# Optimization experiments

Measured on AMD Instinct MI355X. Metric: run time of the kernel, lower is better.

The kernel has to match this reference:

```python
import jax, jax.numpy as jnp
import numpy as np

DT = 0.002  # hardcoded dt0 in SDE.__call__
B, T, D = 4096, 2500, 3


def setup_inputs() -> dict:
    key = jax.random.key(0)
    ks = jax.random.split(key, 6)
    # drift/diffusion scaled by 0.1 so 2500-step Euler paths stay numerically stable in fp32
    return {
        "x0": jax.random.normal(ks[0], (B, D), jnp.float32),
        "drift": jax.random.normal(ks[1], (D, D), jnp.float32) * 0.1,
        "drift_bias": jax.random.normal(ks[2], (D,), jnp.float32),
        "diffusion": jax.random.normal(ks[3], (D, D), jnp.float32) * 0.1,
        "diffusion_bias": jax.random.normal(ks[4], (D,), jnp.float32) * 0.1,
        # standard-normal Brownian increments (scaled by sqrt(dt) inside reference)
        "noise": jax.random.normal(ks[5], (T, B, D), jnp.float32),
    }


def reference(x0, drift, drift_bias, diffusion, diffusion_bias, noise):
    # Euler-Maruyama: x_{k+1} = x_k + (A x_k + b) dt + diag(C x_k + d) dW_k
    # (diag(v) @ dW == v * dW elementwise), vmapped over batch via broadcasting.
    dt = jnp.asarray(DT, x0.dtype)
    sqrt_dt = jnp.sqrt(dt)

    def step(x, eps):
        dW = sqrt_dt * eps                       # [B, D]
        x_new = x + (x @ drift.T + drift_bias) * dt \
                + (x @ diffusion.T + diffusion_bias) * dW
        return x_new, x_new

    _, ys = jax.lax.scan(step, x0, noise)        # ys: [T, B, D]
    paths = jnp.concatenate([x0[None], ys], axis=0)  # [T+1, B, D], SaveAt includes t0
    return jnp.transpose(paths, (1, 0, 2))       # [B, T+1, D] like vmapped sol.ys
```

## Files before the change

### kernel.cpp

```cpp
#include <hip/hip_runtime.h>
#include <math.h>


constexpr int B_N  = 4096;
constexpr int T_N  = 2500;
constexpr int L    = 50;
constexpr int NC   = T_N / L;
constexpr int FL   = 10;
constexpr int NFL  = L / FL;
constexpr int ROWF = (T_N + 1) * 3;

constexpr size_t TRANS_FLOATS = (size_t)NC * B_N * 12;
constexpr size_t BND_OFF      = TRANS_FLOATS;

__global__ __launch_bounds__(64)
void sde_chunk_transforms(const float* __restrict__ A,
                          const float* __restrict__ bv,
                          const float* __restrict__ C,
                          const float* __restrict__ dv,
                          const float* __restrict__ noise,
                          float* __restrict__ trans)
{
    const int b = blockIdx.x * 64 + threadIdx.x;
    const int c = blockIdx.y;

    const float dt  = 0.002f;
    const float sdt = sqrtf(dt);

    float IA[3][3], Cs[3][3], bdt[3], ds[3];
#pragma unroll
    for (int i = 0; i < 3; ++i) {
        bdt[i] = bv[i] * dt;
        ds[i]  = dv[i] * sdt;
#pragma unroll
        for (int j = 0; j < 3; ++j) {
            IA[i][j] = A[i * 3 + j] * dt + (i == j ? 1.0f : 0.0f);
            Cs[i][j] = C[i * 3 + j] * sdt;
        }
    }

    float M[3][3] = {{1,0,0},{0,1,0},{0,0,1}};
    float v[3] = {0, 0, 0};

    const float* __restrict__ nb = noise + (size_t)c * L * (B_N * 3) + (size_t)b * 3;
    const size_t nstride = (size_t)B_N * 3;

    float bufA[FL][3], bufB[FL][3];

    auto loadChunk = [&](float (&buf)[FL][3], int s) {
#pragma unroll
        for (int k = 0; k < FL; ++k) {
            const float* p = nb + ((size_t)s * FL + k) * nstride;
            buf[k][0] = p[0];
            buf[k][1] = p[1];
            buf[k][2] = p[2];
        }
    };

    auto compChunk = [&](const float (&buf)[FL][3]) {
#pragma unroll
        for (int k = 0; k < FL; ++k) {
            const float e[3] = { buf[k][0], buf[k][1], buf[k][2] };
            float S[3][3], t[3];
#pragma unroll
            for (int i = 0; i < 3; ++i) {
                t[i] = fmaf(e[i], ds[i], bdt[i]);
#pragma unroll
                for (int j = 0; j < 3; ++j)
                    S[i][j] = fmaf(e[i], Cs[i][j], IA[i][j]);
            }
            float nM[3][3], nv[3];
#pragma unroll
            for (int i = 0; i < 3; ++i) {
#pragma unroll
                for (int j = 0; j < 3; ++j)
                    nM[i][j] = fmaf(S[i][2], M[2][j], fmaf(S[i][1], M[1][j], S[i][0] * M[0][j]));
                nv[i] = fmaf(S[i][2], v[2], fmaf(S[i][1], v[1], S[i][0] * v[0])) + t[i];
            }
#pragma unroll
            for (int i = 0; i < 3; ++i) {
                v[i] = nv[i];
#pragma unroll
                for (int j = 0; j < 3; ++j) M[i][j] = nM[i][j];
            }
        }
    };

    loadChunk(bufA, 0);
    for (int s = 0; s < NFL; s += 2) {
        if (s + 1 < NFL) loadChunk(bufB, s + 1);
        compChunk(bufA);
        if (s + 2 < NFL) loadChunk(bufA, s + 2);
        if (s + 1 < NFL) compChunk(bufB);
    }

    float* tp = trans + ((size_t)c * B_N + b) * 12;
    float4 w0 = { M[0][0], M[0][1], M[0][2], M[1][0] };
    float4 w1 = { M[1][1], M[1][2], M[2][0], M[2][1] };
    float4 w2 = { M[2][2], v[0],    v[1],    v[2]    };
    ((float4*)tp)[0] = w0;
    ((float4*)tp)[1] = w1;
    ((float4*)tp)[2] = w2;
}

__global__ __launch_bounds__(64)
void sde_scan(const float* __restrict__ x0,
              const float* __restrict__ trans,
              float* __restrict__ bnd,
              float* __restrict__ out)
{
    const int b = blockIdx.x * 64 + threadIdx.x;

    float x[3] = { x0[b * 3 + 0], x0[b * 3 + 1], x0[b * 3 + 2] };

    float* op = out + (size_t)b * ROWF;
    op[0] = x[0]; op[1] = x[1]; op[2] = x[2];

    const float4* tp0 = (const float4*)(trans + (size_t)b * 12);
    const size_t cstride4 = (size_t)B_N * 3;

    float4 a0 = tp0[0], a1 = tp0[1], a2 = tp0[2];

    for (int c = 0; c < NC; ++c) {
        float4 b0, b1, b2;
        if (c + 1 < NC) {
            const float4* tn = tp0 + (size_t)(c + 1) * cstride4;
            b0 = tn[0]; b1 = tn[1]; b2 = tn[2];
        }

        float* bp = bnd + ((size_t)c * B_N + b) * 4;
        ((float4*)bp)[0] = make_float4(x[0], x[1], x[2], 0.0f);

        const float n0 = fmaf(a0.x, x[0], fmaf(a0.y, x[1], fmaf(a0.z, x[2], a2.y)));
        const float n1 = fmaf(a0.w, x[0], fmaf(a1.x, x[1], fmaf(a1.y, x[2], a2.z)));
        const float n2 = fmaf(a1.z, x[0], fmaf(a1.w, x[1], fmaf(a2.x, x[2], a2.w)));
        x[0] = n0; x[1] = n1; x[2] = n2;

        a0 = b0; a1 = b1; a2 = b2;
    }
}

__global__ __launch_bounds__(256)
void sde_replay(const float* __restrict__ A,
                const float* __restrict__ bv,
                const float* __restrict__ C,
                const float* __restrict__ dv,
                const float* __restrict__ noise,
                const float* __restrict__ bnd,
                float* __restrict__ out)
{
    __shared__ float lds[4][64][31];

    const int widx = threadIdx.x >> 6;
    const int lane = threadIdx.x & 63;
    const int wg   = blockIdx.x * 4 + widx;
    const int pg   = wg & 63;
    const int c    = wg >> 6;
    const int b    = (pg << 6) | lane;

    const float dt  = 0.002f;
    const float sdt = sqrtf(dt);

    float Adt[3][3], Cs[3][3], bdt[3], dsv[3];
#pragma unroll
    for (int i = 0; i < 3; ++i) {
        bdt[i] = bv[i] * dt;
        dsv[i] = dv[i] * sdt;
#pragma unroll
        for (int j = 0; j < 3; ++j) {
            Adt[i][j] = A[i * 3 + j] * dt;
            Cs[i][j]  = C[i * 3 + j] * sdt;
        }
    }

    const float4 xb = *(const float4*)(bnd + ((size_t)c * B_N + b) * 4);
    float x0r = xb.x, x1r = xb.y, x2r = xb.z;

    const float* __restrict__ nb = noise + (size_t)c * L * (B_N * 3) + (size_t)b * 3;
    const size_t nstride = (size_t)B_N * 3;

    float (*tile)[31] = lds[widx];

    const int  half = lane >> 5;
    const int  r    = lane & 31;
    const bool act  = r < 30;
    float* __restrict__ sb = out + (size_t)((pg << 6) + half) * ROWF
                                 + (size_t)(c * L + 1) * 3 + r;

    float bufA[FL][3], bufB[FL][3];

    auto loadChunk = [&](float (&buf)[FL][3], int s) {
#pragma unroll
        for (int k = 0; k < FL; ++k) {
            const float* p = nb + ((size_t)s * FL + k) * nstride;
            buf[k][0] = p[0];
            buf[k][1] = p[1];
            buf[k][2] = p[2];
        }
    };

    auto doFlush = [&](const float (&buf)[FL][3], int fl) {
        float st[FL][3];
#pragma unroll
        for (int k = 0; k < FL; ++k) {
            const float e0 = buf[k][0], e1 = buf[k][1], e2 = buf[k][2];

            const float a0 = fmaf(Adt[0][2], x2r, fmaf(Adt[0][1], x1r, fmaf(Adt[0][0], x0r, bdt[0])));
            const float a1 = fmaf(Adt[1][2], x2r, fmaf(Adt[1][1], x1r, fmaf(Adt[1][0], x0r, bdt[1])));
            const float a2 = fmaf(Adt[2][2], x2r, fmaf(Adt[2][1], x1r, fmaf(Adt[2][0], x0r, bdt[2])));

            const float c0 = fmaf(Cs[0][2], x2r, fmaf(Cs[0][1], x1r, fmaf(Cs[0][0], x0r, dsv[0])));
            const float c1 = fmaf(Cs[1][2], x2r, fmaf(Cs[1][1], x1r, fmaf(Cs[1][0], x0r, dsv[1])));
            const float c2 = fmaf(Cs[2][2], x2r, fmaf(Cs[2][1], x1r, fmaf(Cs[2][0], x0r, dsv[2])));

            const float n0 = fmaf(c0, e0, x0r + a0);
            const float n1 = fmaf(c1, e1, x1r + a1);
            const float n2 = fmaf(c2, e2, x2r + a2);

            st[k][0] = n0; st[k][1] = n1; st[k][2] = n2;
            x0r = n0; x1r = n1; x2r = n2;
        }

        asm volatile("s_waitcnt lgkmcnt(0)" ::: "memory");

#pragma unroll
        for (int k = 0; k < FL; ++k) {
            tile[lane][k * 3 + 0] = st[k][0];
            tile[lane][k * 3 + 1] = st[k][1];
            tile[lane][k * 3 + 2] = st[k][2];
        }

        asm volatile("s_waitcnt lgkmcnt(0)" ::: "memory");
        __builtin_amdgcn_sched_barrier(0);

        if (act) {
#pragma unroll
            for (int i = 0; i < 32; ++i) {
                const float val = tile[2 * i + half][r];
                sb[(size_t)(2 * i) * ROWF + fl * (FL * 3)] = val;
            }
        }
    };

    loadChunk(bufA, 0);
    loadChunk(bufB, 1);
    doFlush(bufA, 0);
    loadChunk(bufA, 2);
    doFlush(bufB, 1);
    loadChunk(bufB, 3);
    doFlush(bufA, 2);
    loadChunk(bufA, 4);
    doFlush(bufB, 3);
    doFlush(bufA, 4);
}

extern "C" void kernel_launch(void* const* d_in, const int* in_sizes, int n_in,
                              void* d_out, int out_size, void* d_ws, size_t ws_size,
                              hipStream_t stream) {
    const float* x0    = (const float*)d_in[0];
    const float* A     = (const float*)d_in[1];
    const float* bv    = (const float*)d_in[2];
    const float* C     = (const float*)d_in[3];
    const float* dv    = (const float*)d_in[4];
    const float* noise = (const float*)d_in[5];
    float* out = (float*)d_out;

    float* trans = (float*)d_ws;
    float* bnd   = trans + BND_OFF;

    dim3 gridPC(B_N / 64, NC);

    sde_chunk_transforms<<<gridPC, 64, 0, stream>>>(A, bv, C, dv, noise, trans);
    sde_scan<<<B_N / 64, 64, 0, stream>>>(x0, trans, bnd, out);
    sde_replay<<<(B_N / 64) * NC / 4, 256, 0, stream>>>(A, bv, C, dv, noise, bnd, out);
}
```

Baseline: 95.72 us.

## Store chunk boundaries in place over transforms, use nontemporal IO, shrink replay blocks

The scan now writes each chunk's boundary state into the first float4 of that chunk's transform slot, after that slot has been read, so the separate boundary buffer disappears. The replay kernel switches from 256-thread blocks holding four waves to single-wave 64-thread blocks. It also uses nontemporal loads for noise and nontemporal stores for the output. The aim is a smaller workspace footprint and less cache pollution from streaming data. The in-place overwrite depends on the read-before-write order within each thread.

```diff
diff --git a/kernel.cpp b/kernel.cpp
--- a/kernel.cpp
+++ b/kernel.cpp
@@ -9,9 +9,6 @@
 constexpr int FL   = 10;
 constexpr int NFL  = L / FL;
 constexpr int ROWF = (T_N + 1) * 3;
-
-constexpr size_t TRANS_FLOATS = (size_t)NC * B_N * 12;
-constexpr size_t BND_OFF      = TRANS_FLOATS;
 
 __global__ __launch_bounds__(64)
 void sde_chunk_transforms(const float* __restrict__ A,
@@ -105,8 +102,7 @@
 
 __global__ __launch_bounds__(64)
 void sde_scan(const float* __restrict__ x0,
-              const float* __restrict__ trans,
-              float* __restrict__ bnd,
+              float* __restrict__ trans,
               float* __restrict__ out)
 {
     const int b = blockIdx.x * 64 + threadIdx.x;
@@ -116,7 +112,7 @@
     float* op = out + (size_t)b * ROWF;
     op[0] = x[0]; op[1] = x[1]; op[2] = x[2];
 
-    const float4* tp0 = (const float4*)(trans + (size_t)b * 12);
+    float4* tp0 = (float4*)(trans + (size_t)b * 12);
     const size_t cstride4 = (size_t)B_N * 3;
 
     float4 a0 = tp0[0], a1 = tp0[1], a2 = tp0[2];
@@ -128,8 +124,7 @@
             b0 = tn[0]; b1 = tn[1]; b2 = tn[2];
         }
 
-        float* bp = bnd + ((size_t)c * B_N + b) * 4;
-        ((float4*)bp)[0] = make_float4(x[0], x[1], x[2], 0.0f);
+        tp0[(size_t)c * cstride4] = make_float4(x[0], x[1], x[2], 0.0f);
 
         const float n0 = fmaf(a0.x, x[0], fmaf(a0.y, x[1], fmaf(a0.z, x[2], a2.y)));
         const float n1 = fmaf(a0.w, x[0], fmaf(a1.x, x[1], fmaf(a1.y, x[2], a2.z)));
@@ -140,22 +135,20 @@
     }
 }
 
-__global__ __launch_bounds__(256)
+__global__ __launch_bounds__(64)
 void sde_replay(const float* __restrict__ A,
                 const float* __restrict__ bv,
                 const float* __restrict__ C,
                 const float* __restrict__ dv,
                 const float* __restrict__ noise,
-                const float* __restrict__ bnd,
+                const float* __restrict__ trans,
                 float* __restrict__ out)
 {
-    __shared__ float lds[4][64][31];
-
-    const int widx = threadIdx.x >> 6;
+    __shared__ float tile[64][31];
+
     const int lane = threadIdx.x & 63;
-    const int wg   = blockIdx.x * 4 + widx;
-    const int pg   = wg & 63;
-    const int c    = wg >> 6;
+    const int pg   = blockIdx.x & 63;
+    const int c    = blockIdx.x >> 6;
     const int b    = (pg << 6) | lane;
 
     const float dt  = 0.002f;
@@ -173,13 +166,11 @@
         }
     }
 
-    const float4 xb = *(const float4*)(bnd + ((size_t)c * B_N + b) * 4);
+    const float4 xb = *(const float4*)(trans + ((size_t)c * B_N + b) * 12);
     float x0r = xb.x, x1r = xb.y, x2r = xb.z;
 
     const float* __restrict__ nb = noise + (size_t)c * L * (B_N * 3) + (size_t)b * 3;
     const size_t nstride = (size_t)B_N * 3;
-
-    float (*tile)[31] = lds[widx];
 
     const int  half = lane >> 5;
     const int  r    = lane & 31;
@@ -193,9 +184,9 @@
 #pragma unroll
         for (int k = 0; k < FL; ++k) {
             const float* p = nb + ((size_t)s * FL + k) * nstride;
-            buf[k][0] = p[0];
-            buf[k][1] = p[1];
-            buf[k][2] = p[2];
+            buf[k][0] = __builtin_nontemporal_load(p + 0);
+            buf[k][1] = __builtin_nontemporal_load(p + 1);
+            buf[k][2] = __builtin_nontemporal_load(p + 2);
         }
     };
 
@@ -237,7 +228,7 @@
 #pragma unroll
             for (int i = 0; i < 32; ++i) {
                 const float val = tile[2 * i + half][r];
-                sb[(size_t)(2 * i) * ROWF + fl * (FL * 3)] = val;
+                __builtin_nontemporal_store(val, sb + (size_t)(2 * i) * ROWF + fl * (FL * 3));
             }
         }
     };
@@ -266,11 +257,10 @@
     float* out = (float*)d_out;
 
     float* trans = (float*)d_ws;
-    float* bnd   = trans + BND_OFF;
 
     dim3 gridPC(B_N / 64, NC);
 
     sde_chunk_transforms<<<gridPC, 64, 0, stream>>>(A, bv, C, dv, noise, trans);
-    sde_scan<<<B_N / 64, 64, 0, stream>>>(x0, trans, bnd, out);
-    sde_replay<<<(B_N / 64) * NC / 4, 256, 0, stream>>>(A, bv, C, dv, noise, bnd, out);
-}
+    sde_scan<<<B_N / 64, 64, 0, stream>>>(x0, trans, out);
+    sde_replay<<<64 * NC, 64, 0, stream>>>(A, bv, C, dv, noise, trans, out);
+}
```

Measured after the change: 158.2 us. 65.3% more time.
